# Optimization experiments

Hardware: AMD Instinct MI355X
Metric: run time of the kernel (lower is better)

## Reference

```python
import jax, jax.numpy as jnp
import numpy as np
from jax import lax

T, K, F = 262144, 20, 16


def setup_inputs() -> dict:
    key = jax.random.key(0)
    k1, k2, k3, k4 = jax.random.split(key, 4)
    return {
        "observations": jax.random.normal(k1, (T, F), dtype=jnp.float32),
        "beta_logits": jax.random.normal(k2, (K,), dtype=jnp.float32),
        "pi_logits": jax.random.normal(k3, (K, K), dtype=jnp.float32),
        "means": jax.random.normal(k4, (K, F), dtype=jnp.float32),
        "log_vars": jnp.zeros((K, F), dtype=jnp.float32),
    }


def _stick_breaking(logits):
    b = jax.nn.sigmoid(logits)
    cp = jnp.cumprod(1.0 - b)
    return b * jnp.concatenate([jnp.ones((1,), logits.dtype), cp[:-1]])


def _emission_logp(obs, means, log_vars):
    # Diagonal-covariance MultivariateNormal log_prob, vectorized over T and K
    # without materializing a [T,K,F] intermediate.
    var = jnp.exp(log_vars) + 1e-6                       # [K,F]
    inv = 1.0 / var
    const = jnp.sum(means * means * inv + jnp.log(2.0 * jnp.pi * var), axis=1)  # [K]
    quad = (obs * obs) @ inv.T - 2.0 * (obs @ (means * inv).T)                  # [T,K]
    return -0.5 * (quad + const[None, :])


def reference(observations, beta_logits, pi_logits, means, log_vars):
    w = _stick_breaking(beta_logits)                      # [K]
    P = jax.nn.softmax(pi_logits, axis=1)                 # [K,K]
    em = _emission_logp(observations, means, log_vars)    # [T,K]

    # Forward recursion (normalized alpha, as in the original)
    a0 = w * jnp.exp(em[0])
    a0 = a0 / (a0.sum() + 1e-10)

    def fstep(a, e):
        x = (a @ P) * jnp.exp(e)
        x = x / (x.sum() + 1e-10)
        return x, x

    _, a_rest = lax.scan(fstep, a0, em[1:])
    alpha = jnp.concatenate([a0[None], a_rest], axis=0)   # [T,K]

    # Backward recursion (normalized beta)
    bT = jnp.ones((K,), observations.dtype)

    def bstep(bn, e):
        x = P @ (bn * jnp.exp(e))
        x = x / (x.sum() + 1e-10)
        return x, x

    _, b_rest = lax.scan(bstep, bT, em[1:], reverse=True)
    beta = jnp.concatenate([b_rest, bT[None]], axis=0)    # [T,K]

    log_likelihood = jnp.log(alpha[-1].sum() + 1e-10)
    return alpha, beta, log_likelihood
```

## Files before the change

### kernel.cpp

```cpp
#include <hip/hip_runtime.h>
#include <hip/hip_fp16.h>


namespace {
constexpr int Tn = 262144;
constexpr int Kn = 20;
constexpr int Fn = 16;
constexpr float EPSF = 1e-10f;
constexpr float TINY = 1e-35f;

constexpr int Ln3 = 16;
constexpr int Wn3 = 8;
constexpr int NC3 = Tn / Ln3;
constexpr int NBF8 = NC3 / 2 / 32;
constexpr int NBSC = NC3 / 8;
constexpr int SPC = Ln3 * Kn;

constexpr size_t OFF_E    = 256;
constexpr size_t OFF_MF   = OFF_E + (size_t)Tn*20 + 256;
constexpr size_t OFF_MB   = OFF_MF + (size_t)Tn;
constexpr size_t OFF_MATF = OFF_MB + (size_t)Tn;
constexpr size_t OFF_MATB = OFF_MATF + 4*(size_t)NC3;
constexpr size_t OFF_SF   = OFF_MATB + 4*(size_t)NC3;
constexpr size_t OFF_SB   = OFF_SF + NC3;
constexpr size_t OFF_END  = OFF_SB + NC3;
}

#if __has_builtin(__builtin_amdgcn_rcpf)
#define FRCP(x) __builtin_amdgcn_rcpf(x)
#else
#define FRCP(x) (1.0f/(x))
#endif

template<int CTRL>
__device__ __forceinline__ float dpp_add(float v) {
  int s = __builtin_amdgcn_update_dpp(0, __float_as_int(v), CTRL, 0xF, 0xF, true);
  return v + __int_as_float(s);
}
template<int CTRL>
__device__ __forceinline__ float dppmov(float v) {
  return __int_as_float(__builtin_amdgcn_update_dpp(0, __float_as_int(v), CTRL, 0xF, 0xF, true));
}

__device__ __forceinline__ float reduce8(float v) {
  v = dpp_add<0xB1>(v);
  v = dpp_add<0x4E>(v);
  v = dpp_add<0x141>(v);
  return v;
}

__device__ __forceinline__ unsigned packh2(float a, float b) {
  __half2 h2 = __floats2half2_rn(a, b);
  return *(unsigned*)&h2;
}

__global__ __launch_bounds__(320) void emis_kernel(
    const float* __restrict__ obs, const float* __restrict__ means,
    const float* __restrict__ log_vars, float* ws)
{
  __shared__ __align__(16) float so[64][20];
  __shared__ __align__(16) float scm[16][24];
  __shared__ __align__(16) float scv[16][24];
  __shared__ __align__(16) float sck[20];
  const int tid = threadIdx.x;
  const int t0 = blockIdx.x * 64;

  if (tid < 256) {
    float4 v = ((const float4*)(obs + (size_t)t0 * Fn))[tid];
    int r = tid >> 2, j = tid & 3;
    *(float4*)&so[r][j*4] = v;
  } else {
    int i = tid - 256;
    if (i < Kn) {
      float ck = 0.f;
#pragma unroll
      for (int f = 0; f < Fn; ++f) {
        float lv  = log_vars[i*Fn + f];
        float var = expf(lv) + 1e-6f;
        float iv  = 1.0f / var;
        float mu  = means[i*Fn + f];
        scm[f][i] = mu * iv;
        scv[f][i] = iv;
        ck += mu*mu*iv + logf(6.2831853071795864f * var);
      }
      sck[i] = ck;
    }
  }
  __syncthreads();

  const int tl = tid / 5;
  const int k0 = (tid - tl*5) * 4;

  float o[16];
  *(float4*)&o[0]  = *(const float4*)&so[tl][0];
  *(float4*)&o[4]  = *(const float4*)&so[tl][4];
  *(float4*)&o[8]  = *(const float4*)&so[tl][8];
  *(float4*)&o[12] = *(const float4*)&so[tl][12];

  float s1x=0.f,s1y=0.f,s1z=0.f,s1w=0.f;
  float s2x=0.f,s2y=0.f,s2z=0.f,s2w=0.f;
#pragma unroll
  for (int f = 0; f < Fn; ++f) {
    float4 cm = *(const float4*)&scm[f][k0];
    float4 cv = *(const float4*)&scv[f][k0];
    float ov = o[f];
    s1x = fmaf(cv.x * ov, ov, s1x); s2x = fmaf(cm.x, ov, s2x);
    s1y = fmaf(cv.y * ov, ov, s1y); s2y = fmaf(cm.y, ov, s2y);
    s1z = fmaf(cv.z * ov, ov, s1z); s2z = fmaf(cm.z, ov, s2z);
    s1w = fmaf(cv.w * ov, ov, s1w); s2w = fmaf(cm.w, ov, s2w);
  }
  float4 ckv = *(const float4*)&sck[k0];
  float4 rr;
  rr.x = __expf(fmaf(-0.5f, s1x + ckv.x, s2x));
  rr.y = __expf(fmaf(-0.5f, s1y + ckv.y, s2y));
  rr.z = __expf(fmaf(-0.5f, s1z + ckv.z, s2z));
  rr.w = __expf(fmaf(-0.5f, s1w + ckv.w, s2w));
  *(float4*)(ws + OFF_E + (size_t)(t0 + tl)*20 + k0) = rr;
}

__global__ __launch_bounds__(256) void scan8_kernel(
    const float* __restrict__ beta_logits, const float* __restrict__ pi_logits,
    float* ws, float* out)
{
  __shared__ __align__(16) float Psh[Kn*Kn];
  __shared__ float wsh[Kn];
  const int tid = threadIdx.x;
  if (tid < Kn) {
    float row[Kn]; float mx = -1e30f;
#pragma unroll
    for (int jj = 0; jj < Kn; ++jj) { row[jj] = pi_logits[tid*Kn + jj]; mx = fmaxf(mx, row[jj]); }
    float s = 0.f;
#pragma unroll
    for (int jj = 0; jj < Kn; ++jj) { row[jj] = expf(row[jj] - mx); s += row[jj]; }
    float invs = 1.0f / s;
#pragma unroll
    for (int jj = 0; jj < Kn; ++jj) Psh[tid*Kn + jj] = row[jj] * invs;
  } else if (tid == Kn) {
    float cp = 1.f;
#pragma unroll
    for (int i = 0; i < Kn; ++i) {
      float b = 1.0f / (1.0f + expf(-beta_logits[i]));
      wsh[i] = b * cp;
      cp *= (1.0f - b);
    }
  }
  __syncthreads();

  const int g   = tid >> 3;
  const int j   = tid & 7;
  const int q   = j & 3;
  const int s1i = 8 + j;
  const int s2i = 16 + q;
  const bool isF = ((int)blockIdx.x < NBF8);
  const int pairI = (isF ? (int)blockIdx.x : (int)blockIdx.x - NBF8) * 32 + g;
  const int cA = pairI * 2, cB = cA + 1;
  const float* E = ws + OFF_E;

  float PA0[8], PB0[8], PA1[8], PB1[8], PA2[8], PB2[8];
  float PC0[4], PC1[4], PC2[4];
  {
    const int M[8] = {0,1,2,3,7,6,5,4};
#pragma unroll
    for (int i = 0; i < 8; ++i) {
      int ka = j ^ M[i];
      int kb = 8 + ka;
      if (isF) {
        PA0[i] = Psh[ka*Kn + j];   PB0[i] = Psh[kb*Kn + j];
        PA1[i] = Psh[ka*Kn + s1i]; PB1[i] = Psh[kb*Kn + s1i];
        PA2[i] = Psh[ka*Kn + s2i]; PB2[i] = Psh[kb*Kn + s2i];
      } else {
        PA0[i] = Psh[j*Kn + ka];   PB0[i] = Psh[j*Kn + kb];
        PA1[i] = Psh[s1i*Kn + ka]; PB1[i] = Psh[s1i*Kn + kb];
        PA2[i] = Psh[s2i*Kn + ka]; PB2[i] = Psh[s2i*Kn + kb];
      }
    }
#pragma unroll
    for (int i = 0; i < 4; ++i) {
      int kc = 16 + (q ^ i);
      if (isF) {
        PC0[i] = Psh[kc*Kn + j]; PC1[i] = Psh[kc*Kn + s1i]; PC2[i] = Psh[kc*Kn + s2i];
      } else {
        PC0[i] = Psh[j*Kn + kc]; PC1[i] = Psh[s1i*Kn + kc]; PC2[i] = Psh[s2i*Kn + kc];
      }
    }
  }
  const float w0c = wsh[j], w1c = wsh[s1i], w2c = wsh[s2i];

  float MaA=1.f, McA=0.f, MdA=1.f, MaB=1.f, McB=0.f, MdB=1.f;
  float* mArr = ws + (isF ? OFF_MF : OFF_MB);
  unsigned* uSA = (unsigned*)(out + (isF ? (size_t)0 : (size_t)Tn * Kn) + (size_t)cA * SPC);
  unsigned* uSB = uSA + SPC;

  auto mobius = [&](float m, float& Ma, float& Mc, float& Md) {
    float na = m * Ma;
    float nc = fmaf(EPSF, Mc, na);
    float nd = EPSF * Md;
    float mx = fmaxf(nc, nd);
    float lam = (mx > 0.f) ? FRCP(mx) : 1.0f;
    Ma = na*lam; Mc = nc*lam; Md = nd*lam;
  };
  auto xmv = [&](float w0, float w1, float w2, float& r0, float& r1, float& r2) {
    float x10 = dppmov<0xB1>(w0),  x11 = dppmov<0xB1>(w1),  x12 = dppmov<0xB1>(w2);
    float x20 = dppmov<0x4E>(w0),  x21 = dppmov<0x4E>(w1),  x22 = dppmov<0x4E>(w2);
    float x30 = dppmov<0x1B>(w0),  x31 = dppmov<0x1B>(w1),  x32 = dppmov<0x1B>(w2);
    float m0  = dppmov<0x141>(w0), m1  = dppmov<0x141>(w1);
    float m01 = dppmov<0xB1>(m0),  m11 = dppmov<0xB1>(m1);
    float m02 = dppmov<0x4E>(m0),  m12 = dppmov<0x4E>(m1);
    float m03 = dppmov<0x1B>(m0),  m13 = dppmov<0x1B>(m1);
#define ACC3(PA, PB, PC, OUT)                                             \
    {                                                                     \
      float a  = w0 * PA[0],  b = x10 * PA[1];                            \
      a = fmaf(x20, PA[2], a); b = fmaf(x30, PA[3], b);                   \
      a = fmaf(m0,  PA[4], a); b = fmaf(m01, PA[5], b);                   \
      a = fmaf(m02, PA[6], a); b = fmaf(m03, PA[7], b);                   \
      a = fmaf(w1,  PB[0], a); b = fmaf(x11, PB[1], b);                   \
      a = fmaf(x21, PB[2], a); b = fmaf(x31, PB[3], b);                   \
      a = fmaf(m1,  PB[4], a); b = fmaf(m11, PB[5], b);                   \
      a = fmaf(m12, PB[6], a); b = fmaf(m13, PB[7], b);                   \
      a = fmaf(w2,  PC[0], a); b = fmaf(x12, PC[1], b);                   \
      a = fmaf(x22, PC[2], a); b = fmaf(x32, PC[3], b);                   \
      OUT = a + b;                                                        \
    }
    ACC3(PA0, PB0, PC0, r0)
    ACC3(PA1, PB1, PC1, r1)
    ACC3(PA2, PB2, PC2, r2)
#undef ACC3
  };

  if (isF) {
    const int bSA = cA * Ln3;
    const bool c0 = (cA == 0);
    float vA0, vA1, vA2, vB0, vB1, vB2;
    {
      const float* p0 = E + (ptrdiff_t)(bSA - 8) * 20;
      vA0 = 0.05f * p0[j]; vA1 = 0.05f * p0[s1i]; vA2 = 0.05f * p0[s2i];
      const float* p1 = E + (ptrdiff_t)(bSA + 8) * 20;
      vB0 = 0.05f * p1[j]; vB1 = 0.05f * p1[s1i]; vB2 = 0.05f * p1[s2i];
    }
    float svA = reduce8(fmaf(0.5f, vA2, vA0 + vA1));
    float iVA = (svA > TINY) ? FRCP(svA) : 1.0f;
    if (svA <= TINY) { vA0 = vA1 = vA2 = 0.05f; }
    float AA = svA * iVA;
    float rhoA = (svA > TINY) ? FRCP(svA) : 1.0f;
    float svB = reduce8(fmaf(0.5f, vB2, vB0 + vB1));
    float iVB = (svB > TINY) ? FRCP(svB) : 1.0f;
    if (svB <= TINY) { vB0 = vB1 = vB2 = 0.05f; }
    float AB = svB * iVB;
    float rhoB = (svB > TINY) ? FRCP(svB) : 1.0f;

    const float* pA = E + (ptrdiff_t)(bSA - 7) * 20;
    float eA0a = pA[j], eA1a = pA[s1i], eA2a = pA[s2i]; pA += 20;
    float eA0b = pA[j], eA1b = pA[s1i], eA2b = pA[s2i]; pA += 20;
    float eA0c = pA[j], eA1c = pA[s1i], eA2c = pA[s2i]; pA += 20;
    const float* pB = E + (ptrdiff_t)(bSA + 9) * 20;
    float eB0a = pB[j], eB1a = pB[s1i], eB2a = pB[s2i]; pB += 20;
    float eB0b = pB[j], eB1b = pB[s1i], eB2b = pB[s2i]; pB += 20;
    float eB0c = pB[j], eB1c = pB[s1i], eB2c = pB[s2i]; pB += 20;

    for (int i = 0; i < 23; ++i) {
      const int t = bSA - 7 + i;
      float accA0, accA1, accA2, accB0, accB1, accB2;
      xmv(vA0, vA1, vA2, accA0, accA1, accA2);
      xmv(vB0, vB1, vB2, accB0, accB1, accB2);
      float ea0 = eA0a, ea1 = eA1a, ea2 = eA2a;
      float eb0 = eB0a, eb1 = eB1a, eb2 = eB2a;
      eA0a = eA0b; eA0b = eA0c; eA0c = pA[j];
      eA1a = eA1b; eA1b = eA1c; eA1c = pA[s1i];
      eA2a = eA2b; eA2b = eA2c; eA2c = pA[s2i]; pA += 20;
      eB0a = eB0b; eB0b = eB0c; eB0c = pB[j];
      eB1a = eB1b; eB1b = eB1c; eB1c = pB[s1i];
      eB2a = eB2b; eB2b = eB2c; eB2c = pB[s2i]; pB += 20;
      const bool init0 = c0 && (t == 0);
      vA0 = init0 ? (w0c * ea0) : (accA0 * (ea0 * rhoA));
      vA1 = init0 ? (w1c * ea1) : (accA1 * (ea1 * rhoA));
      vA2 = init0 ? (w2c * ea2) : (accA2 * (ea2 * rhoA));
      vB0 = accB0 * (eb0 * rhoB);
      vB1 = accB1 * (eb1 * rhoB);
      vB2 = accB2 * (eb2 * rhoB);
      float sA = reduce8(fmaf(0.5f, vA2, vA0 + vA1));
      float sB = reduce8(fmaf(0.5f, vB2, vB0 + vB1));
      float mnA = sA * (init0 ? 1.0f : AA);
      float mnB = sB * AB;
      float iVnA = (sA > TINY) ? FRCP(sA) : 1.0f;
      float iVnB = (sB > TINY) ? FRCP(sB) : 1.0f;
      if (sA <= TINY) { vA0 = vA1 = vA2 = 0.05f; }
      if (sB <= TINY) { vB0 = vB1 = vB2 = 0.05f; }
      if (i >= 7) {
        const int lt = i - 7;
        mArr[t] = mnA;
        mArr[t + 16] = mnB;
        mobius(mnA, MaA, McA, MdA);
        mobius(mnB, MaB, McB, MdB);
        uSA[lt*12 + j] = packh2(vA0 * iVnA, vA1 * iVnA);
        uSA[lt*12 + 8 + q] = packh2(vA2 * iVnA, 0.f);
        uSB[lt*12 + j] = packh2(vB0 * iVnB, vB1 * iVnB);
        uSB[lt*12 + 8 + q] = packh2(vB2 * iVnB, 0.f);
      }
      AA = mnA * iVnA; AB = mnB * iVnB;
      rhoA = (mnA > TINY) ? FRCP(mnA) : 1.0f;
      rhoB = (mnB > TINY) ? FRCP(mnB) : 1.0f;
    }
    ((float4*)(ws + OFF_MATF))[cA] = make_float4(MaA, McA, MdA, 0.f);
    ((float4*)(ws + OFF_MATF))[cB] = make_float4(MaB, McB, MdB, 0.f);
  } else {
    const int topA = cA * Ln3 + Ln3 - 1;
    const bool lastB = (cB == NC3 - 1);
    float vA0 = 0.05f, vA1 = 0.05f, vA2 = 0.05f;
    float vB0 = 0.05f, vB1 = 0.05f, vB2 = 0.05f;
    float svA = reduce8(fmaf(0.5f, vA2, vA0 + vA1));
    float AA = (svA > TINY) ? FRCP(svA) : 1.0f;
    float rhoA = 1.0f;
    float AB = AA;
    float rhoB = 1.0f;

    const float* pA = E + (ptrdiff_t)(topA + 8) * 20;
    float eA0a = pA[j], eA1a = pA[s1i], eA2a = pA[s2i]; pA -= 20;
    float eA0b = pA[j], eA1b = pA[s1i], eA2b = pA[s2i]; pA -= 20;
    float eA0c = pA[j], eA1c = pA[s1i], eA2c = pA[s2i]; pA -= 20;
    const float* pB = E + (ptrdiff_t)(topA + 24) * 20;
    float eB0a = pB[j], eB1a = pB[s1i], eB2a = pB[s2i]; pB -= 20;
    float eB0b = pB[j], eB1b = pB[s1i], eB2b = pB[s2i]; pB -= 20;
    float eB0c = pB[j], eB1c = pB[s1i], eB2c = pB[s2i]; pB -= 20;

    for (int i = 0; i < 23; ++i) {
      const int r = topA + 7 - i;
      const bool initB = lastB && ((r + 16) == Tn - 2);
      float wA0 = vA0 * eA0a, wA1 = vA1 * eA1a, wA2 = vA2 * eA2a;
      float vb0 = initB ? 0.05f : vB0;
      float vb1 = initB ? 0.05f : vB1;
      float vb2 = initB ? 0.05f : vB2;
      float wB0 = vb0 * eB0a, wB1 = vb1 * eB1a, wB2 = vb2 * eB2a;
      float accA0, accA1, accA2, accB0, accB1, accB2;
      xmv(wA0, wA1, wA2, accA0, accA1, accA2);
      xmv(wB0, wB1, wB2, accB0, accB1, accB2);
      float rhoBe = initB ? 1.0f : rhoB;
      vA0 = accA0 * rhoA; vA1 = accA1 * rhoA; vA2 = accA2 * rhoA;
      vB0 = accB0 * rhoBe; vB1 = accB1 * rhoBe; vB2 = accB2 * rhoBe;
      eA0a = eA0b; eA0b = eA0c; eA0c = pA[j];
      eA1a = eA1b; eA1b = eA1c; eA1c = pA[s1i];
      eA2a = eA2b; eA2b = eA2c; eA2c = pA[s2i]; pA -= 20;
      eB0a = eB0b; eB0b = eB0c; eB0c = pB[j];
      eB1a = eB1b; eB1b = eB1c; eB1c = pB[s1i];
      eB2a = eB2b; eB2b = eB2c; eB2c = pB[s2i]; pB -= 20;
      float sA = reduce8(fmaf(0.5f, vA2, vA0 + vA1));
      float sB = reduce8(fmaf(0.5f, vB2, vB0 + vB1));
      float mnA = sA * AA;
      float mnB = sB * (initB ? 1.0f : AB);
      float iVnA = (sA > TINY) ? FRCP(sA) : 1.0f;
      float iVnB = (sB > TINY) ? FRCP(sB) : 1.0f;
      if (sA <= TINY) { vA0 = vA1 = vA2 = 0.05f; }
      if (sB <= TINY) { vB0 = vB1 = vB2 = 0.05f; }
      if (i >= 7) {
        const int lr = 22 - i;
        mArr[r + 1] = mnA;
        mobius(mnA, MaA, McA, MdA);
        uSA[lr*12 + j] = packh2(vA0 * iVnA, vA1 * iVnA);
        uSA[lr*12 + 8 + q] = packh2(vA2 * iVnA, 0.f);
        if (!lastB || i >= 8) {
          mArr[r + 17] = mnB;
          mobius(mnB, MaB, McB, MdB);
          uSB[lr*12 + j] = packh2(vB0 * iVnB, vB1 * iVnB);
          uSB[lr*12 + 8 + q] = packh2(vB2 * iVnB, 0.f);
        }
      }
      AA = mnA * iVnA; AB = mnB * iVnB;
      rhoA = (mnA > TINY) ? FRCP(mnA) : 1.0f;
      rhoB = (mnB > TINY) ? FRCP(mnB) : 1.0f;
    }
    ((float4*)(ws + OFF_MATB))[NC3 - 1 - cA] = make_float4(MaA, McA, MdA, 0.f);
    ((float4*)(ws + OFF_MATB))[NC3 - 1 - cB] = make_float4(MaB, McB, MdB, 0.f);
  }
}

__global__ __launch_bounds__(1024) void combine4_kernel(float* ws, float* out)
{
  __shared__ float wag[16][3];
  __shared__ float wpre[16][3];
  const bool isF = (blockIdx.x == 0);
  const float4* M4 = (const float4*)(ws + (isF ? OFF_MATF : OFF_MATB));
  float* sArr = ws + (isF ? OFF_SF : OFF_SB);
  const float s0 = isF ? 1.0f : 20.0f;
  constexpr int PG = NC3 / 1024;
  const int tid  = threadIdx.x;
  const int lane = tid & 63;
  const int wid  = tid >> 6;

  float4 mm[PG];
#pragma unroll
  for (int i = 0; i < PG; ++i) mm[i] = M4[tid*PG + i];

  float a = 1.f, cc = 0.f, d = 1.f;
#pragma unroll
  for (int i = 0; i < PG; ++i) {
    float na = mm[i].x * a;
    float nc = fmaf(mm[i].y, a, mm[i].z * cc);
    float nd = mm[i].z * d;
    float mx = fmaxf(na, fmaxf(nc, nd));
    float lam = (mx > 0.f) ? FRCP(mx) : 1.0f;
    a = na*lam; cc = nc*lam; d = nd*lam;
  }

  float ia = a, ic = cc, id = d;
  for (int off = 1; off < 64; off <<= 1) {
    float pa = __shfl_up(ia, off, 64);
    float pc = __shfl_up(ic, off, 64);
    float pd = __shfl_up(id, off, 64);
    if (lane >= off) {
      float na = ia * pa;
      float nc = fmaf(ic, pa, id * pc);
      float nd = id * pd;
      float mx = fmaxf(na, fmaxf(nc, nd));
      float lam = (mx > 0.f) ? FRCP(mx) : 1.0f;
      ia = na*lam; ic = nc*lam; id = nd*lam;
    }
  }
  if (lane == 63) { wag[wid][0] = ia; wag[wid][1] = ic; wag[wid][2] = id; }
  __syncthreads();

  if (tid == 0) {
    float ea = 1.f, ec = 0.f, ed = 1.f;
#pragma unroll
    for (int w = 0; w < 16; ++w) {
      wpre[w][0] = ea; wpre[w][1] = ec; wpre[w][2] = ed;
      float na = wag[w][0] * ea;
      float nc = fmaf(wag[w][1], ea, wag[w][2] * ec);
      float nd = wag[w][2] * ed;
      float mx = fmaxf(na, fmaxf(nc, nd));
      float lam = (mx > 0.f) ? FRCP(mx) : 1.0f;
      ea = na*lam; ec = nc*lam; ed = nd*lam;
    }
    if (isF) {
      float den = fmaf(ec, s0, ed);
      float sfin = (den > 0.f) ? (ea * s0)/den : 0.f;
      out[(size_t)2 * Tn * Kn] = logf(sfin + EPSF);
    }
  }
  __syncthreads();

  float ea = __shfl_up(ia, 1, 64);
  float ec = __shfl_up(ic, 1, 64);
  float ed = __shfl_up(id, 1, 64);
  if (lane == 0) { ea = 1.f; ec = 0.f; ed = 1.f; }
  float pa = wpre[wid][0], pc = wpre[wid][1], pd = wpre[wid][2];
  float xa = ea * pa;
  float xc = fmaf(ec, pa, ed * pc);
  float xd = ed * pd;

  float num = xa * s0, den = fmaf(xc, s0, xd);
  float s = (den > 0.f) ? num/den : 0.f;
#pragma unroll
  for (int i = 0; i < PG; ++i) {
    sArr[tid*PG + i] = s;
    float nn = mm[i].x * s, dd = fmaf(mm[i].y, s, mm[i].z);
    s = (dd > 0.f) ? nn/dd : 0.f;
  }
}

__global__ __launch_bounds__(128) void scale4_kernel(float* ws, float* out)
{
  const int tid = threadIdx.x;
  const int g   = tid >> 4;
  const int ll  = tid & 15;
  const bool isF = ((int)blockIdx.x < NBSC);
  const int c = (isF ? (int)blockIdx.x : (int)blockIdx.x - NBSC) * 8 + g;
  float* base = out + (isF ? (size_t)0 : (size_t)Tn * Kn) + (size_t)c * SPC;
  const unsigned* uS = (const unsigned*)base;

  float mySig = 1.0f;
  if (isF) {
    const float* mA = ws + OFF_MF;
    float s = ws[OFF_SF + c];
    const int t0 = c * Ln3;
#pragma unroll
    for (int i = 0; i < Ln3; ++i) {
      float z = s * mA[t0 + i];
      float sn = z * FRCP(z + EPSF);
      if (i == ll) mySig = sn;
      s = sn;
    }
  } else {
    const float* mA = ws + OFF_MB;
    float s = ws[OFF_SB + (NC3 - 1 - c)];
    const int top = c * Ln3 + Ln3 - 1;
#pragma unroll
    for (int i = 0; i < Ln3; ++i) {
      int r = top - i;
      float sn;
      if (r == Tn - 1) sn = s;
      else {
        float z = s * mA[r + 1];
        sn = z * FRCP(z + EPSF);
      }
      if (i == Ln3 - 1 - ll) mySig = sn;
      s = sn;
    }
  }

  uint4 ua = ((const uint4*)(uS + ll*12))[0];
  uint4 ub = ((const uint4*)(uS + ll*12))[1];
  uint4 uc = ((const uint4*)(uS + ll*12))[2];
  __syncthreads();

  const bool onesRow = (!isF && c == NC3 - 1 && ll == Ln3 - 1);
  float sg = mySig;
  unsigned slots[12] = {ua.x,ua.y,ua.z,ua.w, ub.x,ub.y,ub.z,ub.w, uc.x,uc.y,uc.z,uc.w};
  float o[20];
#pragma unroll
  for (int jj = 0; jj < 8; ++jj) {
    __half2 h2 = *(__half2*)&slots[jj];
    float2 f2 = __half22float2(h2);
    o[jj]     = f2.x * sg;
    o[8 + jj] = f2.y * sg;
  }
#pragma unroll
  for (int qq = 0; qq < 4; ++qq) {
    __half2 h2 = *(__half2*)&slots[8 + qq];
    float2 f2 = __half22float2(h2);
    o[16 + qq] = f2.x * sg;
  }
  if (onesRow) {
#pragma unroll
    for (int k = 0; k < 20; ++k) o[k] = 1.0f;
  }
  float* dst = base + ll * 20;
  *(float4*)&dst[0]  = *(float4*)&o[0];
  *(float4*)&dst[4]  = *(float4*)&o[4];
  *(float4*)&dst[8]  = *(float4*)&o[8];
  *(float4*)&dst[12] = *(float4*)&o[12];
  *(float4*)&dst[16] = *(float4*)&o[16];
}

extern "C" void kernel_launch(void* const* d_in, const int* in_sizes, int n_in,
                              void* d_out, int out_size, void* d_ws, size_t ws_size,
                              hipStream_t stream) {
  const float* obs         = (const float*)d_in[0];
  const float* beta_logits = (const float*)d_in[1];
  const float* pi_logits   = (const float*)d_in[2];
  const float* means       = (const float*)d_in[3];
  const float* log_vars    = (const float*)d_in[4];
  float* out = (float*)d_out;
  float* ws  = (float*)d_ws;

  hipLaunchKernelGGL(emis_kernel, dim3(Tn/64), dim3(320), 0, stream,
                     obs, means, log_vars, ws);
  hipLaunchKernelGGL(scan8_kernel, dim3(2*NBF8), dim3(256), 0, stream,
                     beta_logits, pi_logits, ws, out);
  hipLaunchKernelGGL(combine4_kernel, dim3(2), dim3(1024), 0, stream, ws, out);
  hipLaunchKernelGGL(scale4_kernel, dim3(2*NBSC), dim3(128), 0, stream, ws, out);
}
```

Before: 93.91 us.

## Halve chunk length in chunked HMM scan to double parallel chunks

Cuts the per-chunk segment length of the parallel forward/backward scan from 16 to 8 steps, so there are twice as many chunks, each running 15 sequential steps (7 warm-up plus 8 kept) instead of 23. The two chunks per lane group now share one emission pointer, and the scale kernel is regrouped to 16 chunks per block. It also adds an occupancy hint to the scan kernel's launch bounds. The sequential critical path per thread shrinks, but the share of redundant warm-up work rises and the combine stage has twice as many chunk matrices to fold.

Result: slower. 278.1 us (+196.1%).

```diff
diff --git a/kernel.cpp b/kernel.cpp
--- a/kernel.cpp
+++ b/kernel.cpp
@@ -9,11 +9,11 @@
 constexpr float EPSF = 1e-10f;
 constexpr float TINY = 1e-35f;
 
-constexpr int Ln3 = 16;
-constexpr int Wn3 = 8;
+constexpr int Ln3 = 8;
 constexpr int NC3 = Tn / Ln3;
 constexpr int NBF8 = NC3 / 2 / 32;
-constexpr int NBSC = NC3 / 8;
+constexpr int NSCG = 16;
+constexpr int NBSC = NC3 / NSCG;
 constexpr int SPC = Ln3 * Kn;
 
 constexpr size_t OFF_E    = 256;
@@ -118,7 +118,7 @@
   *(float4*)(ws + OFF_E + (size_t)(t0 + tl)*20 + k0) = rr;
 }
 
-__global__ __launch_bounds__(256) void scan8_kernel(
+__global__ __launch_bounds__(256, 4) void scan9_kernel(
     const float* __restrict__ beta_logits, const float* __restrict__ pi_logits,
     float* ws, float* out)
 {
@@ -184,12 +184,11 @@
       }
     }
   }
-  const float w0c = wsh[j], w1c = wsh[s1i], w2c = wsh[s2i];
 
   float MaA=1.f, McA=0.f, MdA=1.f, MaB=1.f, McB=0.f, MdB=1.f;
   float* mArr = ws + (isF ? OFF_MF : OFF_MB);
   unsigned* uSA = (unsigned*)(out + (isF ? (size_t)0 : (size_t)Tn * Kn) + (size_t)cA * SPC);
-  unsigned* uSB = uSA + SPC;
+  unsigned* uSB = uSA + (SPC/2) * 3 / 2;
 
   auto mobius = [&](float m, float& Ma, float& Mc, float& Md) {
     float na = m * Ma;
@@ -226,6 +225,10 @@
     ACC3(PA2, PB2, PC2, r2)
 #undef ACC3
   };
+  (void)uSB;
+  unsigned* uA = (unsigned*)(out + (isF ? (size_t)0 : (size_t)Tn * Kn) + (size_t)cA * SPC);
+  unsigned* uB = uA + 2*SPC/2 - SPC/2;
+  uB = (unsigned*)((float*)uA + SPC);
 
   if (isF) {
     const int bSA = cA * Ln3;
@@ -233,9 +236,8 @@
     float vA0, vA1, vA2, vB0, vB1, vB2;
     {
       const float* p0 = E + (ptrdiff_t)(bSA - 8) * 20;
-      vA0 = 0.05f * p0[j]; vA1 = 0.05f * p0[s1i]; vA2 = 0.05f * p0[s2i];
-      const float* p1 = E + (ptrdiff_t)(bSA + 8) * 20;
-      vB0 = 0.05f * p1[j]; vB1 = 0.05f * p1[s1i]; vB2 = 0.05f * p1[s2i];
+      vA0 = 0.05f * p0[j];     vA1 = 0.05f * p0[s1i];     vA2 = 0.05f * p0[s2i];
+      vB0 = 0.05f * p0[160+j]; vB1 = 0.05f * p0[160+s1i]; vB2 = 0.05f * p0[160+s2i];
     }
     float svA = reduce8(fmaf(0.5f, vA2, vA0 + vA1));
     float iVA = (svA > TINY) ? FRCP(svA) : 1.0f;
@@ -248,32 +250,39 @@
     float AB = svB * iVB;
     float rhoB = (svB > TINY) ? FRCP(svB) : 1.0f;
 
-    const float* pA = E + (ptrdiff_t)(bSA - 7) * 20;
-    float eA0a = pA[j], eA1a = pA[s1i], eA2a = pA[s2i]; pA += 20;
-    float eA0b = pA[j], eA1b = pA[s1i], eA2b = pA[s2i]; pA += 20;
-    float eA0c = pA[j], eA1c = pA[s1i], eA2c = pA[s2i]; pA += 20;
-    const float* pB = E + (ptrdiff_t)(bSA + 9) * 20;
-    float eB0a = pB[j], eB1a = pB[s1i], eB2a = pB[s2i]; pB += 20;
-    float eB0b = pB[j], eB1b = pB[s1i], eB2b = pB[s2i]; pB += 20;
-    float eB0c = pB[j], eB1c = pB[s1i], eB2c = pB[s2i]; pB += 20;
-
-    for (int i = 0; i < 23; ++i) {
+    const float* pE = E + (ptrdiff_t)(bSA - 7) * 20;
+    float eA0a = pE[j], eA1a = pE[s1i], eA2a = pE[s2i];
+    float eB0a = pE[160+j], eB1a = pE[160+s1i], eB2a = pE[160+s2i];
+    pE += 20;
+    float eA0b = pE[j], eA1b = pE[s1i], eA2b = pE[s2i];
+    float eB0b = pE[160+j], eB1b = pE[160+s1i], eB2b = pE[160+s2i];
+    pE += 20;
+    float eA0c = pE[j], eA1c = pE[s1i], eA2c = pE[s2i];
+    float eB0c = pE[160+j], eB1c = pE[160+s1i], eB2c = pE[160+s2i];
+    pE += 20;
+
+    for (int i = 0; i < 15; ++i) {
       const int t = bSA - 7 + i;
       float accA0, accA1, accA2, accB0, accB1, accB2;
       xmv(vA0, vA1, vA2, accA0, accA1, accA2);
       xmv(vB0, vB1, vB2, accB0, accB1, accB2);
       float ea0 = eA0a, ea1 = eA1a, ea2 = eA2a;
       float eb0 = eB0a, eb1 = eB1a, eb2 = eB2a;
-      eA0a = eA0b; eA0b = eA0c; eA0c = pA[j];
-      eA1a = eA1b; eA1b = eA1c; eA1c = pA[s1i];
-      eA2a = eA2b; eA2b = eA2c; eA2c = pA[s2i]; pA += 20;
-      eB0a = eB0b; eB0b = eB0c; eB0c = pB[j];
-      eB1a = eB1b; eB1b = eB1c; eB1c = pB[s1i];
-      eB2a = eB2b; eB2b = eB2c; eB2c = pB[s2i]; pB += 20;
-      const bool init0 = c0 && (t == 0);
-      vA0 = init0 ? (w0c * ea0) : (accA0 * (ea0 * rhoA));
-      vA1 = init0 ? (w1c * ea1) : (accA1 * (ea1 * rhoA));
-      vA2 = init0 ? (w2c * ea2) : (accA2 * (ea2 * rhoA));
+      eA0a = eA0b; eA0b = eA0c; eA0c = pE[j];
+      eA1a = eA1b; eA1b = eA1c; eA1c = pE[s1i];
+      eA2a = eA2b; eA2b = eA2c; eA2c = pE[s2i];
+      eB0a = eB0b; eB0b = eB0c; eB0c = pE[160+j];
+      eB1a = eB1b; eB1b = eB1c; eB1c = pE[160+s1i];
+      eB2a = eB2b; eB2b = eB2c; eB2c = pE[160+s2i];
+      pE += 20;
+      const bool init0 = c0 && (i == 7);
+      if (init0) {
+        vA0 = wsh[j] * ea0; vA1 = wsh[s1i] * ea1; vA2 = wsh[s2i] * ea2;
+      } else {
+        vA0 = accA0 * (ea0 * rhoA);
+        vA1 = accA1 * (ea1 * rhoA);
+        vA2 = accA2 * (ea2 * rhoA);
+      }
       vB0 = accB0 * (eb0 * rhoB);
       vB1 = accB1 * (eb1 * rhoB);
       vB2 = accB2 * (eb2 * rhoB);
@@ -288,13 +297,13 @@
       if (i >= 7) {
         const int lt = i - 7;
         mArr[t] = mnA;
-        mArr[t + 16] = mnB;
+        mArr[t + 8] = mnB;
         mobius(mnA, MaA, McA, MdA);
         mobius(mnB, MaB, McB, MdB);
-        uSA[lt*12 + j] = packh2(vA0 * iVnA, vA1 * iVnA);
-        uSA[lt*12 + 8 + q] = packh2(vA2 * iVnA, 0.f);
-        uSB[lt*12 + j] = packh2(vB0 * iVnB, vB1 * iVnB);
-        uSB[lt*12 + 8 + q] = packh2(vB2 * iVnB, 0.f);
+        uA[lt*12 + j] = packh2(vA0 * iVnA, vA1 * iVnA);
+        uA[lt*12 + 8 + q] = packh2(vA2 * iVnA, 0.f);
+        uB[lt*12 + j] = packh2(vB0 * iVnB, vB1 * iVnB);
+        uB[lt*12 + 8 + q] = packh2(vB2 * iVnB, 0.f);
       }
       AA = mnA * iVnA; AB = mnB * iVnB;
       rhoA = (mnA > TINY) ? FRCP(mnA) : 1.0f;
@@ -307,24 +316,25 @@
     const bool lastB = (cB == NC3 - 1);
     float vA0 = 0.05f, vA1 = 0.05f, vA2 = 0.05f;
     float vB0 = 0.05f, vB1 = 0.05f, vB2 = 0.05f;
-    float svA = reduce8(fmaf(0.5f, vA2, vA0 + vA1));
-    float AA = (svA > TINY) ? FRCP(svA) : 1.0f;
+    float AA = 1.0f;
     float rhoA = 1.0f;
-    float AB = AA;
+    float AB = 1.0f;
     float rhoB = 1.0f;
 
-    const float* pA = E + (ptrdiff_t)(topA + 8) * 20;
-    float eA0a = pA[j], eA1a = pA[s1i], eA2a = pA[s2i]; pA -= 20;
-    float eA0b = pA[j], eA1b = pA[s1i], eA2b = pA[s2i]; pA -= 20;
-    float eA0c = pA[j], eA1c = pA[s1i], eA2c = pA[s2i]; pA -= 20;
-    const float* pB = E + (ptrdiff_t)(topA + 24) * 20;
-    float eB0a = pB[j], eB1a = pB[s1i], eB2a = pB[s2i]; pB -= 20;
-    float eB0b = pB[j], eB1b = pB[s1i], eB2b = pB[s2i]; pB -= 20;
-    float eB0c = pB[j], eB1c = pB[s1i], eB2c = pB[s2i]; pB -= 20;
-
-    for (int i = 0; i < 23; ++i) {
+    const float* pE = E + (ptrdiff_t)(topA + 8) * 20;
+    float eA0a = pE[j], eA1a = pE[s1i], eA2a = pE[s2i];
+    float eB0a = pE[160+j], eB1a = pE[160+s1i], eB2a = pE[160+s2i];
+    pE -= 20;
+    float eA0b = pE[j], eA1b = pE[s1i], eA2b = pE[s2i];
+    float eB0b = pE[160+j], eB1b = pE[160+s1i], eB2b = pE[160+s2i];
+    pE -= 20;
+    float eA0c = pE[j], eA1c = pE[s1i], eA2c = pE[s2i];
+    float eB0c = pE[160+j], eB1c = pE[160+s1i], eB2c = pE[160+s2i];
+    pE -= 20;
+
+    for (int i = 0; i < 15; ++i) {
       const int r = topA + 7 - i;
-      const bool initB = lastB && ((r + 16) == Tn - 2);
+      const bool initB = lastB && (i == 8);
       float wA0 = vA0 * eA0a, wA1 = vA1 * eA1a, wA2 = vA2 * eA2a;
       float vb0 = initB ? 0.05f : vB0;
       float vb1 = initB ? 0.05f : vB1;
@@ -336,12 +346,13 @@
       float rhoBe = initB ? 1.0f : rhoB;
       vA0 = accA0 * rhoA; vA1 = accA1 * rhoA; vA2 = accA2 * rhoA;
       vB0 = accB0 * rhoBe; vB1 = accB1 * rhoBe; vB2 = accB2 * rhoBe;
-      eA0a = eA0b; eA0b = eA0c; eA0c = pA[j];
-      eA1a = eA1b; eA1b = eA1c; eA1c = pA[s1i];
-      eA2a = eA2b; eA2b = eA2c; eA2c = pA[s2i]; pA -= 20;
-      eB0a = eB0b; eB0b = eB0c; eB0c = pB[j];
-      eB1a = eB1b; eB1b = eB1c; eB1c = pB[s1i];
-      eB2a = eB2b; eB2b = eB2c; eB2c = pB[s2i]; pB -= 20;
+      eA0a = eA0b; eA0b = eA0c; eA0c = pE[j];
+      eA1a = eA1b; eA1b = eA1c; eA1c = pE[s1i];
+      eA2a = eA2b; eA2b = eA2c; eA2c = pE[s2i];
+      eB0a = eB0b; eB0b = eB0c; eB0c = pE[160+j];
+      eB1a = eB1b; eB1b = eB1c; eB1c = pE[160+s1i];
+      eB2a = eB2b; eB2b = eB2c; eB2c = pE[160+s2i];
+      pE -= 20;
       float sA = reduce8(fmaf(0.5f, vA2, vA0 + vA1));
       float sB = reduce8(fmaf(0.5f, vB2, vB0 + vB1));
       float mnA = sA * AA;
@@ -351,16 +362,16 @@
       if (sA <= TINY) { vA0 = vA1 = vA2 = 0.05f; }
       if (sB <= TINY) { vB0 = vB1 = vB2 = 0.05f; }
       if (i >= 7) {
-        const int lr = 22 - i;
+        const int lr = 14 - i;
         mArr[r + 1] = mnA;
         mobius(mnA, MaA, McA, MdA);
-        uSA[lr*12 + j] = packh2(vA0 * iVnA, vA1 * iVnA);
-        uSA[lr*12 + 8 + q] = packh2(vA2 * iVnA, 0.f);
+        uA[lr*12 + j] = packh2(vA0 * iVnA, vA1 * iVnA);
+        uA[lr*12 + 8 + q] = packh2(vA2 * iVnA, 0.f);
         if (!lastB || i >= 8) {
-          mArr[r + 17] = mnB;
+          mArr[r + 9] = mnB;
           mobius(mnB, MaB, McB, MdB);
-          uSB[lr*12 + j] = packh2(vB0 * iVnB, vB1 * iVnB);
-          uSB[lr*12 + 8 + q] = packh2(vB2 * iVnB, 0.f);
+          uB[lr*12 + j] = packh2(vB0 * iVnB, vB1 * iVnB);
+          uB[lr*12 + 8 + q] = packh2(vB2 * iVnB, 0.f);
         }
       }
       AA = mnA * iVnA; AB = mnB * iVnB;
@@ -456,13 +467,13 @@
   }
 }
 
-__global__ __launch_bounds__(128) void scale4_kernel(float* ws, float* out)
+__global__ __launch_bounds__(128) void scale5_kernel(float* ws, float* out)
 {
   const int tid = threadIdx.x;
-  const int g   = tid >> 4;
-  const int ll  = tid & 15;
+  const int g   = tid >> 3;
+  const int ll  = tid & 7;
   const bool isF = ((int)blockIdx.x < NBSC);
-  const int c = (isF ? (int)blockIdx.x : (int)blockIdx.x - NBSC) * 8 + g;
+  const int c = (isF ? (int)blockIdx.x : (int)blockIdx.x - NBSC) * NSCG + g;
   float* base = out + (isF ? (size_t)0 : (size_t)Tn * Kn) + (size_t)c * SPC;
   const unsigned* uS = (const unsigned*)base;
 
@@ -543,8 +554,8 @@
 
   hipLaunchKernelGGL(emis_kernel, dim3(Tn/64), dim3(320), 0, stream,
                      obs, means, log_vars, ws);
-  hipLaunchKernelGGL(scan8_kernel, dim3(2*NBF8), dim3(256), 0, stream,
+  hipLaunchKernelGGL(scan9_kernel, dim3(2*NBF8), dim3(256), 0, stream,
                      beta_logits, pi_logits, ws, out);
   hipLaunchKernelGGL(combine4_kernel, dim3(2), dim3(1024), 0, stream, ws, out);
-  hipLaunchKernelGGL(scale4_kernel, dim3(2*NBSC), dim3(128), 0, stream, ws, out);
-}
+  hipLaunchKernelGGL(scale5_kernel, dim3(2*NBSC), dim3(128), 0, stream, ws, out);
+}
```
